# Kernel optimization log

Hardware: AMD Instinct MI355X
Metric: run time of the kernel (lower is better)

Reference implementation:

```python
import jax, jax.numpy as jnp
import numpy as np

N = 4096
INPUT_DIM = 512
H1 = 256
H2 = 64
ALPHA = 0.2
MASK_VAL = -9e15


def setup_inputs() -> dict:
    key = jax.random.key(0)
    ks = jax.random.split(key, 10)

    def glorot(k, fan_in, fan_out):
        r = np.sqrt(6.0 / (fan_in + fan_out)).astype(np.float32)
        return jax.random.uniform(k, (fan_in, fan_out), jnp.float32, -r, r)

    return {
        "X": jax.random.normal(ks[0], (N, INPUT_DIM), jnp.float32),
        "adj": jax.random.randint(ks[1], (N, N), 0, 2, jnp.int32),
        "noise": jax.random.normal(ks[2], (N, H2), jnp.float32),
        "W0": glorot(ks[3], INPUT_DIM, H1),
        "a0": jax.random.normal(ks[4], (2 * H1, 1), jnp.float32) * 0.1,
        "W1": glorot(ks[5], H1, H2),
        "a1": jax.random.normal(ks[6], (2 * H2, 1), jnp.float32) * 0.1,
        "W2": glorot(ks[7], H1, H2),
        "a2": jax.random.normal(ks[8], (2 * H2, 1), jnp.float32) * 0.1,
    }


def gat_layer(X, W, a, adj):
    # h: [N, d]
    h = X @ W
    d = h.shape[1]
    # e_ij = leakyrelu(a^T [h_i ; h_j]) == leakyrelu(f1_i + f2_j)
    f1 = h @ a[:d]            # [N, 1]
    f2 = h @ a[d:]            # [N, 1]
    e = jax.nn.leaky_relu(f1 + f2.T, negative_slope=ALPHA)  # [N, N]
    e = jnp.where(adj > 0, e, MASK_VAL)
    attn = jax.nn.softmax(e, axis=1)  # dropout omitted (eval mode)
    return attn @ h


def reference(X, adj, noise, W0, a0, W1, a1, W2, a2):
    hidden = gat_layer(X, W0, a0, adj)
    mean = gat_layer(hidden, W1, a1, adj)
    logstd = gat_layer(hidden, W2, a2, adj)
    Z = noise * jnp.exp(logstd) + mean          # [N, H2]
    A_pred = jax.nn.sigmoid(Z @ Z.T)            # [N, N]
    return A_pred
```

## Files before the change

### kernel.cpp

```cpp
#include <hip/hip_runtime.h>
#include <hip/hip_bf16.h>
#include <math.h>

#define N_NODES 4096
#define DIM_IN  512
#define DH1     256
#define DH2     64
#define ALPHA   0.2f
#define ROW_WORDS (N_NODES / 64)
#define NWORDS  (N_NODES * ROW_WORDS)
#define L2E     1.4426950408889634f

typedef __bf16 bf16_t;
typedef bf16_t bf16x8 __attribute__((ext_vector_type(8)));
typedef float  f32x4  __attribute__((ext_vector_type(4)));


__global__ __launch_bounds__(256) void prep_kernel(
    const float* __restrict__ X, const float* __restrict__ W0,
    const float* __restrict__ W1, const float* __restrict__ W2,
    const int* __restrict__ adj,
    bf16_t* __restrict__ Xb, bf16_t* __restrict__ W0T,
    bf16_t* __restrict__ W12T, unsigned long long* __restrict__ mask,
    float* __restrict__ f1b, float* __restrict__ f2b)
{
    const int b = blockIdx.x;
    const int tid = threadIdx.x;
    if (b < 2048) {
        int i = b * 256 + tid;
        float4 v = ((const float4*)X)[i];
        bf16_t o[4] = {(bf16_t)v.x, (bf16_t)v.y, (bf16_t)v.z, (bf16_t)v.w};
        const int e = i * 4;
        const int row = e >> 9, k = e & 511;
        const size_t base = ((size_t)(row >> 4) * 64 + (k >> 3)) * 128 + (row & 15) * 8 + (k & 7);
        *(uint2*)(Xb + base) = *(const uint2*)o;
    } else if (b < 2560) {
        int o = (b - 2048) * 256 + tid;
        int n = o >> 9, k = o & 511;
        const size_t base = ((size_t)(n >> 4) * 64 + (k >> 3)) * 128 + (n & 15) * 8 + (k & 7);
        W0T[base] = (bf16_t)W0[(size_t)k * DH1 + n];
    } else if (b < 2688) {
        int o = (b - 2560) * 256 + tid;
        int n = o >> 8, k = o & 255;
        const float* W = (n < 64) ? W1 : W2;
        const size_t base = ((size_t)(n >> 4) * 32 + (k >> 3)) * 128 + (n & 15) * 8 + (k & 7);
        W12T[base] = (bf16_t)W[(size_t)k * 64 + (n & 63)];
    } else if (b < 4736) {
        const int lane = tid & 63;
        int gw = ((b - 2688) * 256 + tid) >> 6;
        for (int w = gw; w < NWORDS; w += 8192) {
            int v = adj[(size_t)w * 64 + lane];
            unsigned long long bb = __ballot(v > 0);
            if (lane == 0) mask[w] = bb;
        }
    } else {
        int zb = b - 4736;
        float4* dst = (float4*)((zb < 8) ? f1b : f2b);
        dst[(zb & 7) * 256 + tid] = float4{0.f, 0.f, 0.f, 0.f};
    }
}

__global__ __launch_bounds__(256) void rowstats_kernel(
    const unsigned long long* __restrict__ mask,
    const float* __restrict__ f1b, const float* __restrict__ f2b,
    float* __restrict__ mrowb, float* __restrict__ srowb)
{
    __shared__ float f2s[N_NODES];
    const int l = blockIdx.y;
    const float* f1 = f1b + (size_t)l * N_NODES;
    const float* f2 = f2b + (size_t)l * N_NODES;
    const int tid = threadIdx.x;
    #pragma unroll
    for (int j = 0; j < N_NODES / 4; j += 256)
        ((float4*)f2s)[j + tid] = ((const float4*)f2)[j + tid];
    __syncthreads();
    const int wave = tid >> 6, lane = tid & 63;
    const int row = blockIdx.x * 4 + wave;
    const float fi = f1[row];
    const int l5 = lane & 31;
    const bool lohalf = (lane < 32);

    const unsigned long long wv = mask[(size_t)row * ROW_WORDS + lane];
    const unsigned wlo = (unsigned)wv, whi = (unsigned)(wv >> 32);

    float mx = -3.0e38f;
    #pragma unroll
    for (int t = 0; t < ROW_WORDS; ++t) {
        const unsigned blo = __shfl(wlo, t), bhi = __shfl(whi, t);
        const unsigned sel = lohalf ? blo : bhi;
        if ((sel >> l5) & 1u) {
            float e = fi + f2s[t * 64 + lane];
            e = fmaxf(e, ALPHA * e);
            mx = fmaxf(mx, e);
        }
    }
    for (int off = 32; off; off >>= 1) mx = fmaxf(mx, __shfl_xor(mx, off));

    float sum = 0.f;
    if (mx > -2.0e38f) {
        #pragma unroll
        for (int t = 0; t < ROW_WORDS; ++t) {
            const unsigned blo = __shfl(wlo, t), bhi = __shfl(whi, t);
            const unsigned sel = lohalf ? blo : bhi;
            if ((sel >> l5) & 1u) {
                float e = fi + f2s[t * 64 + lane];
                e = fmaxf(e, ALPHA * e);
                sum += __expf(e - mx);
            }
        }
    }
    for (int off = 32; off; off >>= 1) sum += __shfl_xor(sum, off);
    if (lane == 0) {
        if (mx > -2.0e38f) { mrowb[l * N_NODES + row] = mx; srowb[l * N_NODES + row] = sum; }
        else               { mrowb[l * N_NODES + row] = 0.f; srowb[l * N_NODES + row] = 0.f; }
    }
}

template <int NT, int KLEN>
__global__ __launch_bounds__(256) void attn_fused_kernel(
    const unsigned long long* __restrict__ maskw,
    const float* __restrict__ f1, const float* __restrict__ f2,
    const float* __restrict__ mrow, const float* __restrict__ srow,
    const bf16_t* __restrict__ BT, float* __restrict__ outP, int N)
{
    __shared__ float f2s[KLEN];
    __shared__ float tile[64 * (NT * 16 + 4)];
    const int tid = threadIdx.x;
    const int wave = tid >> 6, lane = tid & 63, quad = lane >> 4, l16 = lane & 15;
    const int colBase = blockIdx.x * (NT * 16);
    const int rowBase = blockIdx.y * 64;
    const int kBeg = blockIdx.z * KLEN;
    const int r = rowBase + wave * 16 + l16;

    if (tid < KLEN / 4) ((float4*)f2s)[tid] = *(const float4*)(f2 + kBeg + tid * 4);

    const float m = mrow[r], s = srow[r];
    const bool uni = (s <= 0.f);
    const float Cr = uni ? 0.f : (-m * L2E - __log2f(s));
    const float f1r = f1[r];
    const float puni = 1.0f / (float)N_NODES;

    __syncthreads();

    const int ubase = (colBase >> 4) * (N_NODES * 16) + kBeg * 16;
    const int laneo = quad * 128 + l16 * 8;
    const int qs = quad * 8;
    const unsigned long long* mptr = maskw + (size_t)r * ROW_WORDS + (kBeg >> 6);

    f32x4 acc[NT] = {};
    unsigned long long mcur = mptr[0];
    for (int w = 0; w < KLEN / 64; ++w) {
        unsigned long long mnext = (w < KLEN / 64 - 1) ? mptr[w + 1] : 0ull;
        const unsigned mlo = (unsigned)mcur, mhi = (unsigned)(mcur >> 32);
        #pragma unroll
        for (int h = 0; h < 2; ++h) {
            const int k0 = w * 64 + h * 32;
            bf16x8 bv[NT];
            #pragma unroll
            for (int t = 0; t < NT; ++t)
                bv[t] = *(const bf16x8*)(BT + ubase + t * (N_NODES * 16) + k0 * 16 + laneo);
            const unsigned bits = ((h ? mhi : mlo) >> qs) & 0xFFu;
            const int kc = k0 + qs;
            bf16x8 av;
            #pragma unroll
            for (int j = 0; j < 8; ++j) {
                float x = f1r + f2s[kc + j];
                float e = fmaxf(x, ALPHA * x);
                float p = ((bits >> j) & 1u) ? exp2f(__builtin_fmaf(e, L2E, Cr)) : 0.f;
                av[j] = (bf16_t)(uni ? puni : p);
            }
            #pragma unroll
            for (int t = 0; t < NT; ++t)
                acc[t] = __builtin_amdgcn_mfma_f32_16x16x32_bf16(av, bv[t], acc[t], 0, 0, 0);
        }
        mcur = mnext;
    }

    #pragma unroll
    for (int t = 0; t < NT; ++t) {
        const int col = t * 16 + l16;
        #pragma unroll
        for (int rr = 0; rr < 4; ++rr)
            tile[(wave * 16 + quad * 4 + rr) * (NT * 16 + 4) + col] = acc[t][rr];
    }
    __syncthreads();
    const int half = lane >> 5, c32 = (lane & 31) * 4;
    float* outBase = outP + (size_t)blockIdx.z * N_NODES * N + (size_t)rowBase * N + colBase;
    #pragma unroll
    for (int p = 0; p < 8; ++p) {
        const int rl = p * 8 + wave * 2 + half;
        f32x4 v = *(const f32x4*)&tile[rl * (NT * 16 + 4) + c32];
        __builtin_nontemporal_store(v, (f32x4*)(outBase + (size_t)rl * N + c32));
    }
}

template <int KLEN>
__global__ __launch_bounds__(256) void attn12_kernel(
    const unsigned long long* __restrict__ maskw,
    const float* __restrict__ f1b, const float* __restrict__ f2b,
    const float* __restrict__ mrowb, const float* __restrict__ srowb,
    const bf16_t* __restrict__ h12T, float* __restrict__ outP)
{
    __shared__ float f2s[KLEN];
    __shared__ float tile[64 * 68];
    const int l = blockIdx.x;
    const float* f1 = f1b + (size_t)l * N_NODES;
    const float* f2 = f2b + (size_t)l * N_NODES;

    const int tid = threadIdx.x;
    const int wave = tid >> 6, lane = tid & 63, quad = lane >> 4, l16 = lane & 15;
    const int rowBase = blockIdx.y * 64;
    const int kBeg = blockIdx.z * KLEN;
    const int r = rowBase + wave * 16 + l16;

    if (tid < KLEN / 4) ((float4*)f2s)[tid] = *(const float4*)(f2 + kBeg + tid * 4);

    const float m = mrowb[l * N_NODES + r], s = srowb[l * N_NODES + r];
    const bool uni = (s <= 0.f);
    const float Cr = uni ? 0.f : (-m * L2E - __log2f(s));
    const float f1r = f1[r];
    const float puni = 1.0f / (float)N_NODES;

    __syncthreads();

    const int ubase = (l * 4) * (N_NODES * 16) + kBeg * 16;
    const int laneo = quad * 128 + l16 * 8;
    const int qs = quad * 8;
    const unsigned long long* mptr = maskw + (size_t)r * ROW_WORDS + (kBeg >> 6);

    f32x4 acc[4] = {};
    unsigned long long mcur = mptr[0];
    for (int w = 0; w < KLEN / 64; ++w) {
        unsigned long long mnext = (w < KLEN / 64 - 1) ? mptr[w + 1] : 0ull;
        const unsigned mlo = (unsigned)mcur, mhi = (unsigned)(mcur >> 32);
        #pragma unroll
        for (int h = 0; h < 2; ++h) {
            const int k0 = w * 64 + h * 32;
            bf16x8 bv[4];
            #pragma unroll
            for (int t = 0; t < 4; ++t)
                bv[t] = *(const bf16x8*)(h12T + ubase + t * (N_NODES * 16) + k0 * 16 + laneo);
            const unsigned bits = ((h ? mhi : mlo) >> qs) & 0xFFu;
            const int kc = k0 + qs;
            bf16x8 av;
            #pragma unroll
            for (int j = 0; j < 8; ++j) {
                float x = f1r + f2s[kc + j];
                float e = fmaxf(x, ALPHA * x);
                float p = ((bits >> j) & 1u) ? exp2f(__builtin_fmaf(e, L2E, Cr)) : 0.f;
                av[j] = (bf16_t)(uni ? puni : p);
            }
            #pragma unroll
            for (int t = 0; t < 4; ++t)
                acc[t] = __builtin_amdgcn_mfma_f32_16x16x32_bf16(av, bv[t], acc[t], 0, 0, 0);
        }
        mcur = mnext;
    }

    #pragma unroll
    for (int t = 0; t < 4; ++t) {
        const int col = t * 16 + l16;
        #pragma unroll
        for (int rr = 0; rr < 4; ++rr)
            tile[(wave * 16 + quad * 4 + rr) * 68 + col] = acc[t][rr];
    }
    __syncthreads();
    const int q4 = lane >> 4, c16 = (lane & 15) * 4;
    float* outBase = outP + ((size_t)blockIdx.z * 2 + l) * (N_NODES * DH2) + (size_t)rowBase * DH2;
    #pragma unroll
    for (int p = 0; p < 4; ++p) {
        const int rl = p * 16 + wave * 4 + q4;
        f32x4 v = *(const f32x4*)&tile[rl * 68 + c16];
        __builtin_nontemporal_store(v, (f32x4*)(outBase + (size_t)rl * DH2 + c16));
    }
}

__global__ __launch_bounds__(256) void reduce_kernel(
    const float* __restrict__ p, bf16_t* __restrict__ out, int n4, int S)
{
    int i = blockIdx.x * 256 + threadIdx.x;
    if (i >= n4) return;
    float4 a = ((const float4*)p)[i];
    for (int s = 1; s < S; ++s) {
        float4 b = ((const float4*)p)[(size_t)s * n4 + i];
        a.x += b.x; a.y += b.y; a.z += b.z; a.w += b.w;
    }
    bf16_t o[4] = {(bf16_t)a.x, (bf16_t)a.y, (bf16_t)a.z, (bf16_t)a.w};
    const int e = i * 4;
    const int row = e >> 8, k = e & 255;
    const size_t base = ((size_t)(row >> 4) * 32 + (k >> 3)) * 128 + (row & 15) * 8 + (k & 7);
    *(uint2*)(out + base) = *(const uint2*)o;
}

__global__ __launch_bounds__(256) void reduce_z_kernel(
    const float* __restrict__ part, const float* __restrict__ noise,
    bf16_t* __restrict__ ZA, bf16_t* __restrict__ ZB)
{
    const int idx = blockIdx.x * 256 + threadIdx.x;
    const int stride = 2 * N_NODES * DH2;
    float mean = 0.f, ls = 0.f;
    #pragma unroll
    for (int s = 0; s < 4; ++s) {
        mean += part[(size_t)s * stride + idx];
        ls   += part[(size_t)s * stride + N_NODES * DH2 + idx];
    }
    float z = noise[idx] * __expf(ls) + mean;
    bf16_t zhi = (bf16_t)z;
    bf16_t zlo = (bf16_t)(z - (float)zhi);
    const int i = idx >> 6, c = idx & 63;
    const size_t base = ((size_t)(i >> 4) * 32 + (c >> 3)) * 128 + (i & 15) * 8 + (c & 7);
    ZA[base]        = zhi;
    ZA[base + 1024] = zhi;
    ZA[base + 2048] = zlo;
    ZA[base + 3072] = zlo;
    ZB[base]        = zhi;
    ZB[base + 1024] = zlo;
    ZB[base + 2048] = zhi;
    ZB[base + 3072] = zlo;
}

template <int NT>
__global__ __launch_bounds__(256) void gemm0_kernel(
    const bf16_t* __restrict__ A, const bf16_t* __restrict__ BT,
    bf16_t* __restrict__ Ct, const float* __restrict__ a0,
    float* __restrict__ f1, float* __restrict__ f2)
{
    const int tid = threadIdx.x;
    const int wave = tid >> 6, lane = tid & 63, quad = lane >> 4, l16 = lane & 15;
    const int colBase = blockIdx.x * (NT * 16), rowBase = blockIdx.y * 64;
    const size_t KS = (size_t)DIM_IN * 16;
    const bf16_t* Ap = A + (size_t)((rowBase >> 4) + wave) * KS + quad * 128 + l16 * 8;
    const bf16_t* Bp = BT + (size_t)(colBase >> 4) * KS + quad * 128 + l16 * 8;

    f32x4 acc[NT] = {};
    for (int k0 = 0; k0 < DIM_IN; k0 += 64) {
        bf16x8 bv[2 * NT];
        #pragma unroll
        for (int t = 0; t < NT; ++t) {
            bv[t]      = *(const bf16x8*)(Bp + (size_t)t * KS + k0 * 16);
            bv[NT + t] = *(const bf16x8*)(Bp + (size_t)t * KS + (k0 + 32) * 16);
        }
        bf16x8 av0 = *(const bf16x8*)(Ap + k0 * 16);
        bf16x8 av1 = *(const bf16x8*)(Ap + (k0 + 32) * 16);
        #pragma unroll
        for (int t = 0; t < NT; ++t)
            acc[t] = __builtin_amdgcn_mfma_f32_16x16x32_bf16(av0, bv[t], acc[t], 0, 0, 0);
        #pragma unroll
        for (int t = 0; t < NT; ++t)
            acc[t] = __builtin_amdgcn_mfma_f32_16x16x32_bf16(av1, bv[NT + t], acc[t], 0, 0, 0);
    }
    #pragma unroll
    for (int t = 0; t < NT; ++t) {
        const int col = colBase + t * 16 + l16;
        bf16_t pk[4];
        #pragma unroll
        for (int rr = 0; rr < 4; ++rr) pk[rr] = (bf16_t)acc[t][rr];
        const int kc = (rowBase + wave * 16 + quad * 4) >> 3;
        const size_t o = ((size_t)(col >> 4) * (N_NODES >> 3) + kc) * 128
                       + (col & 15) * 8 + (quad & 1) * 4;
        *(uint2*)(Ct + o) = *(const uint2*)pk;
    }
    #pragma unroll
    for (int rr = 0; rr < 4; ++rr) {
        float s1 = 0.f, s2 = 0.f;
        #pragma unroll
        for (int t = 0; t < NT; ++t) {
            const int col = colBase + t * 16 + l16;
            s1 += acc[t][rr] * a0[col];
            s2 += acc[t][rr] * a0[DH1 + col];
        }
        #pragma unroll
        for (int off = 8; off; off >>= 1) {
            s1 += __shfl_down(s1, off, 16);
            s2 += __shfl_down(s2, off, 16);
        }
        if (l16 == 0) {
            const int row = rowBase + wave * 16 + quad * 4 + rr;
            atomicAdd(f1 + row, s1);
            atomicAdd(f2 + row, s2);
        }
    }
}

__global__ __launch_bounds__(256) void gemm12_kernel(
    const bf16_t* __restrict__ A, const bf16_t* __restrict__ BT,
    bf16_t* __restrict__ Ct, const float* __restrict__ a1, const float* __restrict__ a2,
    float* __restrict__ f1b, float* __restrict__ f2b)
{
    const int tid = threadIdx.x;
    const int wave = tid >> 6, lane = tid & 63, quad = lane >> 4, l16 = lane & 15;
    const int l = blockIdx.x;
    const int colBase = l * 64, rowBase = blockIdx.y * 64;
    const size_t KS = (size_t)DH1 * 16;
    const bf16_t* Ap = A + (size_t)((rowBase >> 4) + wave) * KS + quad * 128 + l16 * 8;
    const bf16_t* Bp = BT + (size_t)(colBase >> 4) * KS + quad * 128 + l16 * 8;

    f32x4 acc[4] = {};
    for (int k0 = 0; k0 < DH1; k0 += 64) {
        bf16x8 bv[8];
        #pragma unroll
        for (int t = 0; t < 4; ++t) {
            bv[t]     = *(const bf16x8*)(Bp + (size_t)t * KS + k0 * 16);
            bv[4 + t] = *(const bf16x8*)(Bp + (size_t)t * KS + (k0 + 32) * 16);
        }
        bf16x8 av0 = *(const bf16x8*)(Ap + k0 * 16);
        bf16x8 av1 = *(const bf16x8*)(Ap + (k0 + 32) * 16);
        #pragma unroll
        for (int t = 0; t < 4; ++t)
            acc[t] = __builtin_amdgcn_mfma_f32_16x16x32_bf16(av0, bv[t], acc[t], 0, 0, 0);
        #pragma unroll
        for (int t = 0; t < 4; ++t)
            acc[t] = __builtin_amdgcn_mfma_f32_16x16x32_bf16(av1, bv[4 + t], acc[t], 0, 0, 0);
    }
    #pragma unroll
    for (int t = 0; t < 4; ++t) {
        const int col = colBase + t * 16 + l16;
        bf16_t pk[4];
        #pragma unroll
        for (int rr = 0; rr < 4; ++rr) pk[rr] = (bf16_t)acc[t][rr];
        const int kc = (rowBase + wave * 16 + quad * 4) >> 3;
        const size_t o = ((size_t)(col >> 4) * (N_NODES >> 3) + kc) * 128
                       + (col & 15) * 8 + (quad & 1) * 4;
        *(uint2*)(Ct + o) = *(const uint2*)pk;
    }
    const float* a = l ? a2 : a1;
    #pragma unroll
    for (int rr = 0; rr < 4; ++rr) {
        float s1 = 0.f, s2 = 0.f;
        #pragma unroll
        for (int t = 0; t < 4; ++t) {
            const int lc = t * 16 + l16;
            s1 += acc[t][rr] * a[lc];
            s2 += acc[t][rr] * a[64 + lc];
        }
        #pragma unroll
        for (int off = 8; off; off >>= 1) {
            s1 += __shfl_down(s1, off, 16);
            s2 += __shfl_down(s2, off, 16);
        }
        if (l16 == 0) {
            const int row = rowBase + wave * 16 + quad * 4 + rr;
            f1b[l * N_NODES + row] = s1;
            f2b[l * N_NODES + row] = s2;
        }
    }
}

template <int NT>
__global__ __launch_bounds__(256) void zzt_sigmoid_kernel(
    const bf16_t* __restrict__ ZA, const bf16_t* __restrict__ ZB, float* __restrict__ C)
{
    __shared__ float tile[64 * (NT * 16 + 4)];
    const int tid = threadIdx.x;
    const int wave = tid >> 6, lane = tid & 63, quad = lane >> 4, l16 = lane & 15;
    const int colBase = blockIdx.x * (NT * 16), rowBase = blockIdx.y * 64;
    const bf16_t* Ap = ZA + (size_t)((rowBase >> 4) + wave) * 4096 + quad * 128 + l16 * 8;
    const bf16_t* Bp = ZB + (size_t)(colBase >> 4) * 4096 + quad * 128 + l16 * 8;

    f32x4 acc[NT] = {};
    for (int k0 = 0; k0 < 256; k0 += 32) {
        bf16x8 bv[NT];
        #pragma unroll
        for (int t = 0; t < NT; ++t)
            bv[t] = *(const bf16x8*)(Bp + (size_t)t * 4096 + k0 * 16);
        bf16x8 av = *(const bf16x8*)(Ap + k0 * 16);
        #pragma unroll
        for (int t = 0; t < NT; ++t)
            acc[t] = __builtin_amdgcn_mfma_f32_16x16x32_bf16(av, bv[t], acc[t], 0, 0, 0);
    }
    #pragma unroll
    for (int t = 0; t < NT; ++t) {
        const int col = t * 16 + l16;
        #pragma unroll
        for (int rr = 0; rr < 4; ++rr) {
            const int rl = wave * 16 + quad * 4 + rr;
            float x = acc[t][rr];
            tile[rl * (NT * 16 + 4) + col] = __builtin_amdgcn_rcpf(1.0f + exp2f(-x * L2E));
        }
    }
    __syncthreads();
    const int half = lane >> 5, c32 = (lane & 31) * 4;
    float* outBase = C + (size_t)rowBase * N_NODES + colBase;
    #pragma unroll
    for (int p = 0; p < 8; ++p) {
        const int rl = p * 8 + wave * 2 + half;
        f32x4 v = *(const f32x4*)&tile[rl * (NT * 16 + 4) + c32];
        __builtin_nontemporal_store(v, (f32x4*)(outBase + (size_t)rl * N_NODES + c32));
    }
}

extern "C" void kernel_launch(void* const* d_in, const int* in_sizes, int n_in,
                              void* d_out, int out_size, void* d_ws, size_t ws_size,
                              hipStream_t stream)
{
    const float* X     = (const float*)d_in[0];
    const int*   adj   = (const int*)  d_in[1];
    const float* noise = (const float*)d_in[2];
    const float* W0    = (const float*)d_in[3];
    const float* a0    = (const float*)d_in[4];
    const float* W1    = (const float*)d_in[5];
    const float* a1    = (const float*)d_in[6];
    const float* W2    = (const float*)d_in[7];
    const float* a2    = (const float*)d_in[8];
    float* out = (float*)d_out;

    char* ws = (char*)d_ws;
    size_t off = 0;
    auto alloc = [&](size_t bytes) { char* p = ws + off; off += (bytes + 255) & ~(size_t)255; return p; };

    unsigned long long* mask = (unsigned long long*)alloc((size_t)NWORDS * 8);
    float*  part  = (float*)alloc((size_t)4 * N_NODES * DH1 * 4);
    bf16_t* Xb    = (bf16_t*)alloc((size_t)N_NODES * DIM_IN * 2);
    bf16_t* W0T   = (bf16_t*)alloc((size_t)DH1 * DIM_IN * 2);
    bf16_t* W12T  = (bf16_t*)alloc((size_t)128 * DH1 * 2);
    bf16_t* h0T   = (bf16_t*)alloc((size_t)DH1 * N_NODES * 2);
    bf16_t* hidb  = (bf16_t*)alloc((size_t)N_NODES * DH1 * 2);
    bf16_t* h12T  = (bf16_t*)alloc((size_t)128 * N_NODES * 2);
    bf16_t* ZA    = (bf16_t*)alloc((size_t)N_NODES * 256 * 2);
    bf16_t* ZB    = (bf16_t*)alloc((size_t)N_NODES * 256 * 2);
    float* f1b  = (float*)alloc((size_t)2 * N_NODES * 4);
    float* f2b  = (float*)alloc((size_t)2 * N_NODES * 4);
    float* mrowb = (float*)alloc((size_t)2 * N_NODES * 4);
    float* srowb = (float*)alloc((size_t)2 * N_NODES * 4);
    (void)ws_size; (void)in_sizes; (void)n_in; (void)out_size;

    dim3 blk(256);

    prep_kernel<<<4752, blk, 0, stream>>>(X, W0, W1, W2, adj, Xb, W0T, W12T, mask, f1b, f2b);

    gemm0_kernel<2><<<dim3(8, N_NODES / 64), blk, 0, stream>>>(
        Xb, W0T, h0T, a0, f1b, f2b);
    rowstats_kernel<<<dim3(N_NODES / 4, 1), blk, 0, stream>>>(mask, f1b, f2b, mrowb, srowb);
    attn_fused_kernel<8, 1024><<<dim3(2, N_NODES / 64, 4), blk, 0, stream>>>(
        mask, f1b, f2b, mrowb, srowb, h0T, part, DH1);
    reduce_kernel<<<(N_NODES * DH1 / 4 + 255) / 256, blk, 0, stream>>>(
        part, hidb, N_NODES * DH1 / 4, 4);

    gemm12_kernel<<<dim3(2, N_NODES / 64), blk, 0, stream>>>(
        hidb, W12T, h12T, a1, a2, f1b, f2b);

    rowstats_kernel<<<dim3(N_NODES / 4, 2), blk, 0, stream>>>(mask, f1b, f2b, mrowb, srowb);
    attn12_kernel<1024><<<dim3(2, N_NODES / 64, 4), blk, 0, stream>>>(
        mask, f1b, f2b, mrowb, srowb, h12T, part);
    reduce_z_kernel<<<(N_NODES * DH2) / 256, blk, 0, stream>>>(part, noise, ZA, ZB);

    zzt_sigmoid_kernel<8><<<dim3(N_NODES / 128, N_NODES / 64), blk, 0, stream>>>(
        ZA, ZB, out);
}
```

Baseline: 284.0 us.

## Fold softmax row statistics into attention kernels and normalize in reductions

Removes the two rowstats passes that computed each row's max and sum before attention. The attention kernels now compute unnormalized exp(e) directly, accumulate each row's partial sum of probabilities alongside the MFMA product, and write those sums out. The reduce kernels then divide by the combined sum. This saves two launches and a full extra pass over the mask and the exp work. The trade-off is that without max subtraction the exp can overflow for large logits, and rows with no neighbours now produce zeros instead of the uniform-attention fallback.

After: 232.2 us. 1.22x faster.

```diff
diff --git a/kernel.cpp b/kernel.cpp
--- a/kernel.cpp
+++ b/kernel.cpp
@@ -60,68 +60,12 @@
     }
 }
 
-__global__ __launch_bounds__(256) void rowstats_kernel(
-    const unsigned long long* __restrict__ mask,
-    const float* __restrict__ f1b, const float* __restrict__ f2b,
-    float* __restrict__ mrowb, float* __restrict__ srowb)
-{
-    __shared__ float f2s[N_NODES];
-    const int l = blockIdx.y;
-    const float* f1 = f1b + (size_t)l * N_NODES;
-    const float* f2 = f2b + (size_t)l * N_NODES;
-    const int tid = threadIdx.x;
-    #pragma unroll
-    for (int j = 0; j < N_NODES / 4; j += 256)
-        ((float4*)f2s)[j + tid] = ((const float4*)f2)[j + tid];
-    __syncthreads();
-    const int wave = tid >> 6, lane = tid & 63;
-    const int row = blockIdx.x * 4 + wave;
-    const float fi = f1[row];
-    const int l5 = lane & 31;
-    const bool lohalf = (lane < 32);
-
-    const unsigned long long wv = mask[(size_t)row * ROW_WORDS + lane];
-    const unsigned wlo = (unsigned)wv, whi = (unsigned)(wv >> 32);
-
-    float mx = -3.0e38f;
-    #pragma unroll
-    for (int t = 0; t < ROW_WORDS; ++t) {
-        const unsigned blo = __shfl(wlo, t), bhi = __shfl(whi, t);
-        const unsigned sel = lohalf ? blo : bhi;
-        if ((sel >> l5) & 1u) {
-            float e = fi + f2s[t * 64 + lane];
-            e = fmaxf(e, ALPHA * e);
-            mx = fmaxf(mx, e);
-        }
-    }
-    for (int off = 32; off; off >>= 1) mx = fmaxf(mx, __shfl_xor(mx, off));
-
-    float sum = 0.f;
-    if (mx > -2.0e38f) {
-        #pragma unroll
-        for (int t = 0; t < ROW_WORDS; ++t) {
-            const unsigned blo = __shfl(wlo, t), bhi = __shfl(whi, t);
-            const unsigned sel = lohalf ? blo : bhi;
-            if ((sel >> l5) & 1u) {
-                float e = fi + f2s[t * 64 + lane];
-                e = fmaxf(e, ALPHA * e);
-                sum += __expf(e - mx);
-            }
-        }
-    }
-    for (int off = 32; off; off >>= 1) sum += __shfl_xor(sum, off);
-    if (lane == 0) {
-        if (mx > -2.0e38f) { mrowb[l * N_NODES + row] = mx; srowb[l * N_NODES + row] = sum; }
-        else               { mrowb[l * N_NODES + row] = 0.f; srowb[l * N_NODES + row] = 0.f; }
-    }
-}
-
 template <int NT, int KLEN>
 __global__ __launch_bounds__(256) void attn_fused_kernel(
     const unsigned long long* __restrict__ maskw,
     const float* __restrict__ f1, const float* __restrict__ f2,
-    const float* __restrict__ mrow, const float* __restrict__ srow,
-    const bf16_t* __restrict__ BT, float* __restrict__ outP, int N)
+    const bf16_t* __restrict__ BT, float* __restrict__ outP,
+    float* __restrict__ sOut)
 {
     __shared__ float f2s[KLEN];
     __shared__ float tile[64 * (NT * 16 + 4)];
@@ -134,11 +78,7 @@
 
     if (tid < KLEN / 4) ((float4*)f2s)[tid] = *(const float4*)(f2 + kBeg + tid * 4);
 
-    const float m = mrow[r], s = srow[r];
-    const bool uni = (s <= 0.f);
-    const float Cr = uni ? 0.f : (-m * L2E - __log2f(s));
     const float f1r = f1[r];
-    const float puni = 1.0f / (float)N_NODES;
 
     __syncthreads();
 
@@ -148,6 +88,7 @@
     const unsigned long long* mptr = maskw + (size_t)r * ROW_WORDS + (kBeg >> 6);
 
     f32x4 acc[NT] = {};
+    float ssum = 0.f;
     unsigned long long mcur = mptr[0];
     for (int w = 0; w < KLEN / 64; ++w) {
         unsigned long long mnext = (w < KLEN / 64 - 1) ? mptr[w + 1] : 0ull;
@@ -166,8 +107,9 @@
             for (int j = 0; j < 8; ++j) {
                 float x = f1r + f2s[kc + j];
                 float e = fmaxf(x, ALPHA * x);
-                float p = ((bits >> j) & 1u) ? exp2f(__builtin_fmaf(e, L2E, Cr)) : 0.f;
-                av[j] = (bf16_t)(uni ? puni : p);
+                float p = ((bits >> j) & 1u) ? exp2f(e * L2E) : 0.f;
+                ssum += p;
+                av[j] = (bf16_t)p;
             }
             #pragma unroll
             for (int t = 0; t < NT; ++t)
@@ -176,6 +118,11 @@
         mcur = mnext;
     }
 
+    ssum += __shfl_xor(ssum, 16);
+    ssum += __shfl_xor(ssum, 32);
+    if (blockIdx.x == 0 && quad == 0)
+        sOut[(size_t)blockIdx.z * N_NODES + r] = ssum;
+
     #pragma unroll
     for (int t = 0; t < NT; ++t) {
         const int col = t * 16 + l16;
@@ -185,12 +132,12 @@
     }
     __syncthreads();
     const int half = lane >> 5, c32 = (lane & 31) * 4;
-    float* outBase = outP + (size_t)blockIdx.z * N_NODES * N + (size_t)rowBase * N + colBase;
+    float* outBase = outP + (size_t)blockIdx.z * N_NODES * DH1 + (size_t)rowBase * DH1 + colBase;
     #pragma unroll
     for (int p = 0; p < 8; ++p) {
         const int rl = p * 8 + wave * 2 + half;
         f32x4 v = *(const f32x4*)&tile[rl * (NT * 16 + 4) + c32];
-        __builtin_nontemporal_store(v, (f32x4*)(outBase + (size_t)rl * N + c32));
+        __builtin_nontemporal_store(v, (f32x4*)(outBase + (size_t)rl * DH1 + c32));
     }
 }
 
@@ -198,8 +145,8 @@
 __global__ __launch_bounds__(256) void attn12_kernel(
     const unsigned long long* __restrict__ maskw,
     const float* __restrict__ f1b, const float* __restrict__ f2b,
-    const float* __restrict__ mrowb, const float* __restrict__ srowb,
-    const bf16_t* __restrict__ h12T, float* __restrict__ outP)
+    const bf16_t* __restrict__ h12T, float* __restrict__ outP,
+    float* __restrict__ s12)
 {
     __shared__ float f2s[KLEN];
     __shared__ float tile[64 * 68];
@@ -215,11 +162,7 @@
 
     if (tid < KLEN / 4) ((float4*)f2s)[tid] = *(const float4*)(f2 + kBeg + tid * 4);
 
-    const float m = mrowb[l * N_NODES + r], s = srowb[l * N_NODES + r];
-    const bool uni = (s <= 0.f);
-    const float Cr = uni ? 0.f : (-m * L2E - __log2f(s));
     const float f1r = f1[r];
-    const float puni = 1.0f / (float)N_NODES;
 
     __syncthreads();
 
@@ -229,6 +172,7 @@
     const unsigned long long* mptr = maskw + (size_t)r * ROW_WORDS + (kBeg >> 6);
 
     f32x4 acc[4] = {};
+    float ssum = 0.f;
     unsigned long long mcur = mptr[0];
     for (int w = 0; w < KLEN / 64; ++w) {
         unsigned long long mnext = (w < KLEN / 64 - 1) ? mptr[w + 1] : 0ull;
@@ -247,8 +191,9 @@
             for (int j = 0; j < 8; ++j) {
                 float x = f1r + f2s[kc + j];
                 float e = fmaxf(x, ALPHA * x);
-                float p = ((bits >> j) & 1u) ? exp2f(__builtin_fmaf(e, L2E, Cr)) : 0.f;
-                av[j] = (bf16_t)(uni ? puni : p);
+                float p = ((bits >> j) & 1u) ? exp2f(e * L2E) : 0.f;
+                ssum += p;
+                av[j] = (bf16_t)p;
             }
             #pragma unroll
             for (int t = 0; t < 4; ++t)
@@ -257,6 +202,11 @@
         mcur = mnext;
     }
 
+    ssum += __shfl_xor(ssum, 16);
+    ssum += __shfl_xor(ssum, 32);
+    if (quad == 0)
+        s12[((size_t)blockIdx.z * 2 + l) * N_NODES + r] = ssum;
+
     #pragma unroll
     for (int t = 0; t < 4; ++t) {
         const int col = t * 16 + l16;
@@ -276,34 +226,42 @@
 }
 
 __global__ __launch_bounds__(256) void reduce_kernel(
-    const float* __restrict__ p, bf16_t* __restrict__ out, int n4, int S)
-{
+    const float* __restrict__ p, const float* __restrict__ sA, bf16_t* __restrict__ out)
+{
+    const int n4 = N_NODES * DH1 / 4;
     int i = blockIdx.x * 256 + threadIdx.x;
-    if (i >= n4) return;
+    const int e = i * 4;
+    const int row = e >> 8, k = e & 255;
+    float S = sA[row] + sA[N_NODES + row] + sA[2 * N_NODES + row] + sA[3 * N_NODES + row];
+    const float inv = (S > 0.f) ? 1.f / S : 0.f;
     float4 a = ((const float4*)p)[i];
-    for (int s = 1; s < S; ++s) {
+    for (int s = 1; s < 4; ++s) {
         float4 b = ((const float4*)p)[(size_t)s * n4 + i];
         a.x += b.x; a.y += b.y; a.z += b.z; a.w += b.w;
     }
+    a.x *= inv; a.y *= inv; a.z *= inv; a.w *= inv;
     bf16_t o[4] = {(bf16_t)a.x, (bf16_t)a.y, (bf16_t)a.z, (bf16_t)a.w};
-    const int e = i * 4;
-    const int row = e >> 8, k = e & 255;
     const size_t base = ((size_t)(row >> 4) * 32 + (k >> 3)) * 128 + (row & 15) * 8 + (k & 7);
     *(uint2*)(out + base) = *(const uint2*)o;
 }
 
 __global__ __launch_bounds__(256) void reduce_z_kernel(
-    const float* __restrict__ part, const float* __restrict__ noise,
-    bf16_t* __restrict__ ZA, bf16_t* __restrict__ ZB)
+    const float* __restrict__ part, const float* __restrict__ s12,
+    const float* __restrict__ noise, bf16_t* __restrict__ ZA, bf16_t* __restrict__ ZB)
 {
     const int idx = blockIdx.x * 256 + threadIdx.x;
+    const int row = idx >> 6;
     const int stride = 2 * N_NODES * DH2;
-    float mean = 0.f, ls = 0.f;
+    float Sm = 0.f, Sl = 0.f, mean = 0.f, ls = 0.f;
     #pragma unroll
     for (int s = 0; s < 4; ++s) {
+        Sm   += s12[((size_t)s * 2 + 0) * N_NODES + row];
+        Sl   += s12[((size_t)s * 2 + 1) * N_NODES + row];
         mean += part[(size_t)s * stride + idx];
         ls   += part[(size_t)s * stride + N_NODES * DH2 + idx];
     }
+    mean *= (Sm > 0.f) ? 1.f / Sm : 0.f;
+    ls   *= (Sl > 0.f) ? 1.f / Sl : 0.f;
     float z = noise[idx] * __expf(ls) + mean;
     bf16_t zhi = (bf16_t)z;
     bf16_t zlo = (bf16_t)(z - (float)zhi);
@@ -520,8 +478,8 @@
     bf16_t* ZB    = (bf16_t*)alloc((size_t)N_NODES * 256 * 2);
     float* f1b  = (float*)alloc((size_t)2 * N_NODES * 4);
     float* f2b  = (float*)alloc((size_t)2 * N_NODES * 4);
-    float* mrowb = (float*)alloc((size_t)2 * N_NODES * 4);
-    float* srowb = (float*)alloc((size_t)2 * N_NODES * 4);
+    float* sA   = (float*)alloc((size_t)4 * N_NODES * 4);
+    float* s12  = (float*)alloc((size_t)4 * 2 * N_NODES * 4);
     (void)ws_size; (void)in_sizes; (void)n_in; (void)out_size;
 
     dim3 blk(256);
@@ -530,19 +488,16 @@
 
     gemm0_kernel<2><<<dim3(8, N_NODES / 64), blk, 0, stream>>>(
         Xb, W0T, h0T, a0, f1b, f2b);
-    rowstats_kernel<<<dim3(N_NODES / 4, 1), blk, 0, stream>>>(mask, f1b, f2b, mrowb, srowb);
     attn_fused_kernel<8, 1024><<<dim3(2, N_NODES / 64, 4), blk, 0, stream>>>(
-        mask, f1b, f2b, mrowb, srowb, h0T, part, DH1);
-    reduce_kernel<<<(N_NODES * DH1 / 4 + 255) / 256, blk, 0, stream>>>(
-        part, hidb, N_NODES * DH1 / 4, 4);
+        mask, f1b, f2b, h0T, part, sA);
+    reduce_kernel<<<1024, blk, 0, stream>>>(part, sA, hidb);
 
     gemm12_kernel<<<dim3(2, N_NODES / 64), blk, 0, stream>>>(
         hidb, W12T, h12T, a1, a2, f1b, f2b);
 
-    rowstats_kernel<<<dim3(N_NODES / 4, 2), blk, 0, stream>>>(mask, f1b, f2b, mrowb, srowb);
     attn12_kernel<1024><<<dim3(2, N_NODES / 64, 4), blk, 0, stream>>>(
-        mask, f1b, f2b, mrowb, srowb, h12T, part);
-    reduce_z_kernel<<<(N_NODES * DH2) / 256, blk, 0, stream>>>(part, noise, ZA, ZB);
+        mask, f1b, f2b, h12T, part, s12);
+    reduce_z_kernel<<<1024, blk, 0, stream>>>(part, s12, noise, ZA, ZB);
 
     zzt_sigmoid_kernel<8><<<dim3(N_NODES / 128, N_NODES / 64), blk, 0, stream>>>(
         ZA, ZB, out);
```
